# Kernel optimization log

Measured on AMD Instinct MI355X. Metric: run time of the kernel, lower is better.

The kernel has to match this reference:

```python
import jax, jax.numpy as jnp
import numpy as np

H = 16
DH = 64
THETA = 10000.0


def setup_inputs() -> dict:
    key = jax.random.key(0)
    ks = jax.random.split(key, 9)
    B, M, R = 4, 1024, 256
    d = H * DH
    s = 0.05
    return {
        "Pq": jax.random.normal(ks[0], (B, M, R), jnp.float32) * s,
        "Pk": jax.random.normal(ks[1], (B, M, R), jnp.float32) * s,
        "Pv": jax.random.normal(ks[2], (B, M, R), jnp.float32) * s,
        "Vq": jax.random.normal(ks[3], (R, d), jnp.float32) * s,
        "Vk": jax.random.normal(ks[4], (R, d), jnp.float32) * s,
        "Vv": jax.random.normal(ks[5], (R, d), jnp.float32) * s,
        "bq": jax.random.normal(ks[6], (d,), jnp.float32) * s,
        "bk": jax.random.normal(ks[7], (d,), jnp.float32) * s,
        "bv": jax.random.normal(ks[8], (d,), jnp.float32) * s,
        "attention_mask": jnp.ones((B, M), jnp.int32),
        "position_ids": jnp.tile(jnp.arange(M, dtype=jnp.int32), (B, 1)),
    }


def _rope_cos_sin(position_ids):
    # half-dim frequencies, matching the kernel's half-half rotation
    half = DH // 2
    inv_freq = 1.0 / (THETA ** (jnp.arange(0, half, dtype=jnp.float32) / half))
    ang = position_ids.astype(jnp.float32)[..., None] * inv_freq  # [B,M,half]
    return jnp.cos(ang), jnp.sin(ang)


def _rotate(x, cos, sin):
    # x: [B,H,M,dh]; cos/sin: [B,M,half] -> broadcast over heads
    half = DH // 2
    x0, x1 = x[..., :half], x[..., half:]
    c = cos[:, None, :, :]
    s = sin[:, None, :, :]
    return jnp.concatenate([x0 * c - x1 * s, x0 * s + x1 * c], axis=-1)


def reference(Pq, Pk, Pv, Vq, Vk, Vv, bq, bk, bv, attention_mask, position_ids):
    B, M, R = Pq.shape
    # reconstruct per-head Q/K/V from low-rank factors
    Vq3 = Vq.reshape(R, H, DH)
    Vk3 = Vk.reshape(R, H, DH)
    Vv3 = Vv.reshape(R, H, DH)
    q = jnp.einsum("bmr,rhd->bhmd", Pq, Vq3) + bq.reshape(H, DH)[None, :, None, :]
    k = jnp.einsum("bmr,rhd->bhmd", Pk, Vk3) + bk.reshape(H, DH)[None, :, None, :]
    v = jnp.einsum("bmr,rhd->bhmd", Pv, Vv3) + bv.reshape(H, DH)[None, :, None, :]
    cos, sin = _rope_cos_sin(position_ids)
    q = _rotate(q, cos, sin)
    k = _rotate(k, cos, sin)
    scale = 1.0 / jnp.sqrt(jnp.float32(DH))
    scores = jnp.einsum("bhmd,bhnd->bhmn", q, k) * scale  # [B,H,M,M]
    valid = attention_mask.astype(bool)
    pad = valid[:, None, :, None] & valid[:, None, None, :]
    scores = jnp.where(pad, scores, -jnp.inf)
    p = jax.nn.softmax(scores, axis=-1)
    out = jnp.einsum("bhmn,bhnd->bhmd", p, v)
    return out
```

## Files before the change

### kernel.cpp

```cpp
#include <hip/hip_runtime.h>
#include <hip/hip_bf16.h>
#include <math.h>

#define BB 4
#define MM 1024
#define RR 256
#define HH 16
#define DHH 64
#define DD (HH*DHH)

typedef __attribute__((ext_vector_type(8))) short short8;
typedef __attribute__((ext_vector_type(4))) float f32x4;

static __device__ __forceinline__ unsigned short f2bf(float x) {
    __hip_bfloat16 h = __float2bfloat16(x);
    return *(unsigned short*)&h;
}

#if defined(__has_builtin)
#  if __has_builtin(__builtin_amdgcn_exp2f)
#    define EXP2F(x) __builtin_amdgcn_exp2f(x)
#  endif
#endif
#ifndef EXP2F
#  define EXP2F(x) __expf((x) * 0.6931471805599453f)
#endif

static __device__ __forceinline__ unsigned pack_bf16_rh(float a, float b) {
    unsigned ua = __builtin_bit_cast(unsigned, a) + 0x8000u;
    unsigned ub = __builtin_bit_cast(unsigned, b) + 0x8000u;
    return __builtin_amdgcn_perm(ub, ua, 0x07060302u);
}

__global__ __launch_bounds__(256) void prep_kernel(
    const float* __restrict__ Vq, const float* __restrict__ Vk, const float* __restrict__ Vv,
    __hip_bfloat16* __restrict__ VTq, __hip_bfloat16* __restrict__ VTk,
    __hip_bfloat16* __restrict__ VTv)
{
    const int t   = threadIdx.x;
    const int z   = blockIdx.x / 256;
    const int rem = blockIdx.x % 256;
    const int r0  = (rem & 7) * 32;
    const int d0  = (rem >> 3) * 32;
    const float* V = (z == 0) ? Vq : (z == 1) ? Vk : Vv;
    __hip_bfloat16* VT = (z == 0) ? VTq : (z == 1) ? VTk : VTv;

    __shared__ __hip_bfloat16 Ts[32][33];
    {
        const int row = t >> 3;
        const int c4  = (t & 7) * 4;
        float4 f = *(const float4*)&V[(size_t)(r0 + row) * DD + d0 + c4];
        Ts[row][c4 + 0] = __float2bfloat16(f.x);
        Ts[row][c4 + 1] = __float2bfloat16(f.y);
        Ts[row][c4 + 2] = __float2bfloat16(f.z);
        Ts[row][c4 + 3] = __float2bfloat16(f.w);
    }
    __syncthreads();
    {
        const int orow = t >> 3;
        const int oc4  = (t & 7) * 4;
        union { unsigned short u[4]; uint2 v; } pk;
        #pragma unroll
        for (int i = 0; i < 4; ++i) pk.u[i] = *(unsigned short*)&Ts[oc4 + i][orow];
        *(uint2*)&VT[(size_t)(d0 + orow) * RR + r0 + oc4] = pk.v;
    }
}

__global__ __launch_bounds__(256) void svd_gemm(
    const float* __restrict__ Pq, const float* __restrict__ Pk, const float* __restrict__ Pv,
    const __hip_bfloat16* __restrict__ VTq, const __hip_bfloat16* __restrict__ VTk,
    const __hip_bfloat16* __restrict__ VTv,
    const float* __restrict__ bq, const float* __restrict__ bk, const float* __restrict__ bv,
    const int* __restrict__ pos_ids,
    __hip_bfloat16* __restrict__ qout, __hip_bfloat16* __restrict__ kout,
    __hip_bfloat16* __restrict__ vTout)
{
    const int which = blockIdx.z;
    const float* P           = (which == 0) ? Pq : (which == 1) ? Pk : Pv;
    const __hip_bfloat16* VT = (which == 0) ? VTq : (which == 1) ? VTk : VTv;
    const float* bias        = (which == 0) ? bq : (which == 1) ? bk : bv;

    const int hg  = blockIdx.y;
    const int bm0 = blockIdx.x * 64;
    const int b   = bm0 >> 10;
    const int m0  = bm0 & 1023;
    const int tid = threadIdx.x;
    const int lane = tid & 63;
    const int w    = tid >> 6;
    const int l15  = lane & 15;
    const int quad = lane >> 4;

    __shared__ alignas(16) short SM[(64 + 256) * 72];
    short* As = SM;
    short* Bs = SM + 64 * 72;

    f32x4 acc[16];
    #pragma unroll
    for (int dt = 0; dt < 16; ++dt) acc[dt] = (f32x4){0.f, 0.f, 0.f, 0.f};

    for (int kc = 0; kc < 4; ++kc) {
        #pragma unroll
        for (int i = 0; i < 4; ++i) {
            int u   = tid + i * 256;
            int row = u >> 4;
            int c4  = (u & 15) * 4;
            float4 f = *(const float4*)&P[(size_t)(bm0 + row) * RR + kc * 64 + c4];
            uint2 pk;
            pk.x = pack_bf16_rh(f.x, f.y);
            pk.y = pack_bf16_rh(f.z, f.w);
            *(uint2*)&As[row * 72 + c4] = pk;
        }
        #pragma unroll
        for (int i = 0; i < 8; ++i) {
            int u   = tid + i * 256;
            int row = u >> 3;
            int cg  = (u & 7) * 8;
            *(uint4*)&Bs[row * 72 + cg] =
                *(const uint4*)((const short*)VT + (size_t)(hg * 256 + row) * RR + kc * 64 + cg);
        }
        __syncthreads();

        #pragma unroll
        for (int ks = 0; ks < 2; ++ks) {
            short8 a = *(const short8*)&As[(w * 16 + l15) * 72 + ks * 32 + quad * 8];
            #pragma unroll
            for (int dt = 0; dt < 16; ++dt) {
                short8 bf = *(const short8*)&Bs[(dt * 16 + l15) * 72 + ks * 32 + quad * 8];
                acc[dt] = __builtin_amdgcn_mfma_f32_16x16x32_bf16(a, bf, acc[dt], 0, 0, 0);
            }
        }
        __syncthreads();
    }

    #pragma unroll
    for (int dt = 0; dt < 16; ++dt) {
        float bc = bias[hg * 256 + dt * 16 + l15];
        #pragma unroll
        for (int r = 0; r < 4; ++r) acc[dt][r] += bc;
    }

    if (which < 2) {
        __hip_bfloat16* out = (which == 0) ? qout : kout;
        int pm[4];
        #pragma unroll
        for (int r = 0; r < 4; ++r)
            pm[r] = pos_ids[bm0 + w * 16 + quad * 4 + r];
        float cB[2][4], sB[2][4];
        #pragma unroll
        for (int f2 = 0; f2 < 2; ++f2) {
            float invf = __powf(10000.0f, -(float)(f2 * 16 + l15) * (1.0f / 32.0f));
            #pragma unroll
            for (int r = 0; r < 4; ++r) {
                float ang = (float)pm[r] * invf;
                __sincosf(ang, &sB[f2][r], &cB[f2][r]);
            }
        }
        #pragma unroll
        for (int dt = 0; dt < 16; ++dt) {
            const int h  = hg * 4 + (dt >> 2);
            const int cd = (dt & 3) * 16 + l15;
            const int f2 = dt & 1;
            #pragma unroll
            for (int r = 0; r < 4; ++r) {
                float x  = acc[dt][r];
                float xp = acc[dt ^ 2][r];
                float c = cB[f2][r], s = sB[f2][r];
                float val = ((dt & 3) < 2) ? (x * c - xp * s) : (xp * s + x * c);
                int m = m0 + w * 16 + quad * 4 + r;
                out[(((size_t)b * HH + h) * MM + m) * DHH + cd] = __float2bfloat16(val);
            }
        }
    } else {
        short* Tt = SM;
        #pragma unroll
        for (int pp = 0; pp < 2; ++pp) {
            __syncthreads();
            #pragma unroll
            for (int dt2 = 0; dt2 < 8; ++dt2) {
                int dt = pp * 8 + dt2;
                uint2 pk;
                pk.x = pack_bf16_rh(acc[dt][0], acc[dt][1]);
                pk.y = pack_bf16_rh(acc[dt][2], acc[dt][3]);
                *(uint2*)&Tt[(dt2 * 16 + l15) * 72 + w * 16 + quad * 4] = pk;
            }
            __syncthreads();
            #pragma unroll
            for (int i = 0; i < 4; ++i) {
                int u   = tid + i * 256;
                int row = u >> 3;
                int seg = u & 7;
                int dl  = pp * 128 + row;
                int h   = hg * 4 + (dl >> 6);
                int din = dl & 63;
                *(uint4*)&vTout[(((size_t)b * HH + h) * DHH + din) * MM + m0 + seg * 8] =
                    *(const uint4*)&Tt[row * 72 + seg * 8];
            }
        }
    }
}

__global__ __launch_bounds__(256, 2) void attn_kernel(
    const __hip_bfloat16* __restrict__ q, const __hip_bfloat16* __restrict__ k,
    const __hip_bfloat16* __restrict__ vT,
    const int* __restrict__ mask, float* __restrict__ out)
{
    const int bh   = blockIdx.x & 63;
    const int qt   = blockIdx.x >> 6;
    const int b    = bh >> 4;
    const int tid  = threadIdx.x;
    const int lane = tid & 63;
    const int w    = tid >> 6;
    const int l15  = lane & 15;
    const int quad = lane >> 4;
    const int q0   = qt * 128;

    __shared__ alignas(16) __hip_bfloat16 Kt[128][72];
    __shared__ alignas(16) __hip_bfloat16 Vt[64][136];

    const short* kbase = (const short*)k  + (size_t)bh * MM * DHH;
    const short* vbase = (const short*)vT + (size_t)bh * DHH * MM;

    short8 qa[2][2];
    #pragma unroll
    for (int mt = 0; mt < 2; ++mt) {
        const short* qb = (const short*)q +
            ((size_t)bh * MM + q0 + w * 32 + mt * 16 + l15) * DHH + quad * 8;
        qa[mt][0] = *(const short8*)(qb);
        qa[mt][1] = *(const short8*)(qb + 32);
    }

    f32x4 Ot[2][4];
    #pragma unroll
    for (int mt = 0; mt < 2; ++mt)
        #pragma unroll
        for (int dt = 0; dt < 4; ++dt) Ot[mt][dt] = (f32x4){0.f, 0.f, 0.f, 0.f};
    float lsum[2] = {0.f, 0.f};

    const int* maskb = mask + b * MM;
    const int srcbase = (lane & 48) | ((lane & 48) >> 2);
    const float k2 = 0.125f * 1.44269504089f;

    for (int nc = 0; nc < MM / 128; ++nc) {
        const int n0 = nc * 128;
        #pragma unroll
        for (int pass = 0; pass < 4; ++pass) {
            int u   = tid + pass * 256;
            int row = u >> 3;
            int cg  = u & 7;
            *(uint4*)&Kt[row][cg * 8] =
                *(const uint4*)(kbase + (size_t)(n0 + row) * DHH + cg * 8);
        }
        #pragma unroll
        for (int pass = 0; pass < 4; ++pass) {
            int u   = tid + pass * 256;
            int row = u >> 4;
            int c   = u & 15;
            union { uint4 q4; uint2 h2[2]; } vld;
            vld.q4 = *(const uint4*)(vbase + (size_t)row * MM + n0 + c * 8);
            int g  = c >> 3;
            int c6 = c & 7;
            int base0 = g * 64 + (c6 >> 2) * 32 + (c6 & 1) * 16 + ((c6 >> 1) & 1) * 4;
            *(uint2*)&Vt[row][base0]     = vld.h2[0];
            *(uint2*)&Vt[row][base0 + 8] = vld.h2[1];
        }
        __syncthreads();

        unsigned long long bal0 = __ballot(maskb[n0 + lane] != 0);
        unsigned long long bal1 = __ballot(maskb[n0 + 64 + lane] != 0);

        f32x4 S[2][8];
        #pragma unroll
        for (int t = 0; t < 8; ++t) {
            const short* kr = (const short*)&Kt[t * 16 + l15][quad * 8];
            short8 ka0 = *(const short8*)(kr);
            short8 ka1 = *(const short8*)(kr + 32);
            #pragma unroll
            for (int mt = 0; mt < 2; ++mt) {
                f32x4 c = (f32x4){0.f, 0.f, 0.f, 0.f};
                c = __builtin_amdgcn_mfma_f32_16x16x32_bf16(ka0, qa[mt][0], c, 0, 0, 0);
                c = __builtin_amdgcn_mfma_f32_16x16x32_bf16(ka1, qa[mt][1], c, 0, 0, 0);
                S[mt][t] = c;
            }
        }

        #pragma unroll
        for (int t = 0; t < 8; ++t) {
            unsigned bits = (unsigned)((t < 4 ? bal0 : bal1) >> ((t & 3) * 16 + quad * 4));
            #pragma unroll
            for (int r = 0; r < 4; ++r) {
                float sb = ((bits >> r) & 1u) ? 0.0f : -1e30f;
                #pragma unroll
                for (int mt = 0; mt < 2; ++mt) {
                    float e = EXP2F(fmaf(S[mt][t][r], k2, sb));
                    lsum[mt] += e;
                    S[mt][t][r] = e;
                }
            }
        }

        short8 pa[2][4];
        #pragma unroll
        for (int mt = 0; mt < 2; ++mt)
            #pragma unroll
            for (int p = 0; p < 4; ++p) {
                union { unsigned u[4]; short8 s; } pk;
                pk.u[0] = pack_bf16_rh(S[mt][2*p][0],   S[mt][2*p][1]);
                pk.u[1] = pack_bf16_rh(S[mt][2*p][2],   S[mt][2*p][3]);
                pk.u[2] = pack_bf16_rh(S[mt][2*p+1][0], S[mt][2*p+1][1]);
                pk.u[3] = pack_bf16_rh(S[mt][2*p+1][2], S[mt][2*p+1][3]);
                pa[mt][p] = pk.s;
            }

        #pragma unroll
        for (int p = 0; p < 4; ++p) {
            #pragma unroll
            for (int dt = 0; dt < 4; ++dt) {
                short8 vb = *(const short8*)&Vt[dt * 16 + l15][p * 32 + quad * 8];
                #pragma unroll
                for (int mt = 0; mt < 2; ++mt)
                    Ot[mt][dt] = __builtin_amdgcn_mfma_f32_16x16x32_bf16(pa[mt][p], vb, Ot[mt][dt], 0, 0, 0);
            }
        }
        __syncthreads();
    }

    #pragma unroll
    for (int mt = 0; mt < 2; ++mt) {
        float s = lsum[mt];
        s += __shfl_xor(s, 16, 64);
        s += __shfl_xor(s, 32, 64);
        float inv = 1.0f / s;
        float* ob = out + ((size_t)bh * MM + q0 + w * 32 + mt * 16) * DHH;
        #pragma unroll
        for (int r = 0; r < 4; ++r) {
            float ir = __shfl(inv, srcbase + r, 64);
            #pragma unroll
            for (int dt = 0; dt < 4; ++dt)
                ob[(quad * 4 + r) * DHH + dt * 16 + l15] = Ot[mt][dt][r] * ir;
        }
    }
}

extern "C" void kernel_launch(void* const* d_in, const int* in_sizes, int n_in,
                              void* d_out, int out_size, void* d_ws, size_t ws_size,
                              hipStream_t stream) {
    const float* Pq = (const float*)d_in[0];
    const float* Pk = (const float*)d_in[1];
    const float* Pv = (const float*)d_in[2];
    const float* Vq = (const float*)d_in[3];
    const float* Vk = (const float*)d_in[4];
    const float* Vv = (const float*)d_in[5];
    const float* bq = (const float*)d_in[6];
    const float* bk = (const float*)d_in[7];
    const float* bv = (const float*)d_in[8];
    const int* mask = (const int*)d_in[9];
    const int* pos  = (const int*)d_in[10];
    float* out = (float*)d_out;

    const size_t qkv_elems = (size_t)BB * HH * MM * DHH;
    __hip_bfloat16* qb  = (__hip_bfloat16*)d_ws;
    __hip_bfloat16* kb  = qb + qkv_elems;
    __hip_bfloat16* vT  = kb + qkv_elems;
    __hip_bfloat16* VTq = vT + qkv_elems;
    __hip_bfloat16* VTk = VTq + (size_t)DD * RR;
    __hip_bfloat16* VTv = VTk + (size_t)DD * RR;

    prep_kernel<<<768, 256, 0, stream>>>(Vq, Vk, Vv, VTq, VTk, VTv);

    dim3 gG(BB * MM / 64, HH / 4, 3);
    svd_gemm<<<gG, 256, 0, stream>>>(Pq, Pk, Pv, VTq, VTk, VTv, bq, bk, bv, pos,
                                     qb, kb, vT);

    attn_kernel<<<BB * HH * (MM / 128), 256, 0, stream>>>(qb, kb, vT, mask, out);
}
```

Baseline: 156.4 us.

## Retile SVD projection GEMM to 128x128 tiles with A operands read straight into registers

Each block of the low-rank Q/K/V projection now covers 128 rows by 128 output columns (two heads) instead of 64 rows by 256 columns. The P operand is loaded from global memory, converted to bf16 and packed directly into MFMA A fragments, with no staging through LDS. Only the V^T tile is staged in shared memory, in two K chunks of 128 with separate accumulators that are summed at the end. The aim is fewer LDS round trips and barriers and more MFMAs per B fragment load. In exchange, each P row is read by twice as many blocks and register use per thread goes up.

```diff
diff --git a/kernel.cpp b/kernel.cpp
--- a/kernel.cpp
+++ b/kernel.cpp
@@ -81,7 +81,7 @@
     const float* bias        = (which == 0) ? bq : (which == 1) ? bk : bv;
 
     const int hg  = blockIdx.y;
-    const int bm0 = blockIdx.x * 64;
+    const int bm0 = blockIdx.x * 128;
     const int b   = bm0 >> 10;
     const int m0  = bm0 & 1023;
     const int tid = threadIdx.x;
@@ -90,111 +90,137 @@
     const int l15  = lane & 15;
     const int quad = lane >> 4;
 
-    __shared__ alignas(16) short SM[(64 + 256) * 72];
-    short* As = SM;
-    short* Bs = SM + 64 * 72;
+    __shared__ alignas(16) short Bs[128 * 136];
 
     f32x4 acc[16];
-    #pragma unroll
-    for (int dt = 0; dt < 16; ++dt) acc[dt] = (f32x4){0.f, 0.f, 0.f, 0.f};
-
-    for (int kc = 0; kc < 4; ++kc) {
-        #pragma unroll
-        for (int i = 0; i < 4; ++i) {
+    f32x4 acc2[16];
+    #pragma unroll
+    for (int dt = 0; dt < 16; ++dt) {
+        acc[dt]  = (f32x4){0.f, 0.f, 0.f, 0.f};
+        acc2[dt] = (f32x4){0.f, 0.f, 0.f, 0.f};
+    }
+
+    const float* prow0 = P + (size_t)(bm0 + w * 32 + l15) * RR;
+    const float* prow1 = P + (size_t)(bm0 + w * 32 + 16 + l15) * RR;
+
+    #pragma unroll
+    for (int kc = 0; kc < 2; ++kc) {
+        #pragma unroll
+        for (int i = 0; i < 8; ++i) {
             int u   = tid + i * 256;
             int row = u >> 4;
-            int c4  = (u & 15) * 4;
-            float4 f = *(const float4*)&P[(size_t)(bm0 + row) * RR + kc * 64 + c4];
+            int cg  = (u & 15) * 8;
+            *(uint4*)&Bs[row * 136 + cg] =
+                *(const uint4*)((const short*)VT + (size_t)(hg * 128 + row) * RR + kc * 128 + cg);
+        }
+        __syncthreads();
+
+        #pragma unroll
+        for (int ks = 0; ks < 4; ++ks) {
+            const int ko = kc * 128 + ks * 32 + quad * 8;
+            float4 a0lo = *(const float4*)(prow0 + ko);
+            float4 a0hi = *(const float4*)(prow0 + ko + 4);
+            float4 a1lo = *(const float4*)(prow1 + ko);
+            float4 a1hi = *(const float4*)(prow1 + ko + 4);
+            union { unsigned u[4]; short8 s; } pa0, pa1;
+            pa0.u[0] = pack_bf16_rh(a0lo.x, a0lo.y);
+            pa0.u[1] = pack_bf16_rh(a0lo.z, a0lo.w);
+            pa0.u[2] = pack_bf16_rh(a0hi.x, a0hi.y);
+            pa0.u[3] = pack_bf16_rh(a0hi.z, a0hi.w);
+            pa1.u[0] = pack_bf16_rh(a1lo.x, a1lo.y);
+            pa1.u[1] = pack_bf16_rh(a1lo.z, a1lo.w);
+            pa1.u[2] = pack_bf16_rh(a1hi.x, a1hi.y);
+            pa1.u[3] = pack_bf16_rh(a1hi.z, a1hi.w);
+
+            #pragma unroll
+            for (int dt = 0; dt < 8; ++dt) {
+                short8 bf = *(const short8*)&Bs[(dt * 16 + l15) * 136 + ks * 32 + quad * 8];
+                acc[kc * 8 + dt]  = __builtin_amdgcn_mfma_f32_16x16x32_bf16(pa0.s, bf, acc[kc * 8 + dt], 0, 0, 0);
+                acc2[kc * 8 + dt] = __builtin_amdgcn_mfma_f32_16x16x32_bf16(pa1.s, bf, acc2[kc * 8 + dt], 0, 0, 0);
+            }
+        }
+        __syncthreads();
+    }
+    #pragma unroll
+    for (int dt = 0; dt < 8; ++dt) {
+        #pragma unroll
+        for (int r = 0; r < 4; ++r) {
+            acc[dt][r]  += acc[8 + dt][r];
+            acc2[dt][r] += acc2[8 + dt][r];
+        }
+    }
+
+    #pragma unroll
+    for (int dt = 0; dt < 8; ++dt) {
+        float bc = bias[hg * 128 + dt * 16 + l15];
+        #pragma unroll
+        for (int r = 0; r < 4; ++r) { acc[dt][r] += bc; acc2[dt][r] += bc; }
+    }
+
+    if (which < 2) {
+        __hip_bfloat16* out = (which == 0) ? qout : kout;
+        int pm0[4], pm1[4];
+        #pragma unroll
+        for (int r = 0; r < 4; ++r) {
+            pm0[r] = pos_ids[bm0 + w * 32 + quad * 4 + r];
+            pm1[r] = pos_ids[bm0 + w * 32 + 16 + quad * 4 + r];
+        }
+        float cB[2][2][4], sB[2][2][4];
+        #pragma unroll
+        for (int f2 = 0; f2 < 2; ++f2) {
+            float invf = __powf(10000.0f, -(float)(f2 * 16 + l15) * (1.0f / 32.0f));
+            #pragma unroll
+            for (int r = 0; r < 4; ++r) {
+                __sincosf((float)pm0[r] * invf, &sB[f2][0][r], &cB[f2][0][r]);
+                __sincosf((float)pm1[r] * invf, &sB[f2][1][r], &cB[f2][1][r]);
+            }
+        }
+        #pragma unroll
+        for (int dt = 0; dt < 8; ++dt) {
+            const int h  = hg * 2 + (dt >> 2);
+            const int cd = (dt & 3) * 16 + l15;
+            const int f2 = dt & 1;
+            #pragma unroll
+            for (int r = 0; r < 4; ++r) {
+                {
+                    float x  = acc[dt][r], xp = acc[dt ^ 2][r];
+                    float c = cB[f2][0][r], s = sB[f2][0][r];
+                    float val = ((dt & 3) < 2) ? (x * c - xp * s) : (xp * s + x * c);
+                    int m = m0 + w * 32 + quad * 4 + r;
+                    out[(((size_t)b * HH + h) * MM + m) * DHH + cd] = __float2bfloat16(val);
+                }
+                {
+                    float x  = acc2[dt][r], xp = acc2[dt ^ 2][r];
+                    float c = cB[f2][1][r], s = sB[f2][1][r];
+                    float val = ((dt & 3) < 2) ? (x * c - xp * s) : (xp * s + x * c);
+                    int m = m0 + w * 32 + 16 + quad * 4 + r;
+                    out[(((size_t)b * HH + h) * MM + m) * DHH + cd] = __float2bfloat16(val);
+                }
+            }
+        }
+    } else {
+        short* Tt = Bs;
+        __syncthreads();
+        #pragma unroll
+        for (int dt = 0; dt < 8; ++dt) {
             uint2 pk;
-            pk.x = pack_bf16_rh(f.x, f.y);
-            pk.y = pack_bf16_rh(f.z, f.w);
-            *(uint2*)&As[row * 72 + c4] = pk;
-        }
+            pk.x = pack_bf16_rh(acc[dt][0], acc[dt][1]);
+            pk.y = pack_bf16_rh(acc[dt][2], acc[dt][3]);
+            *(uint2*)&Tt[(dt * 16 + l15) * 136 + w * 32 + quad * 4] = pk;
+            pk.x = pack_bf16_rh(acc2[dt][0], acc2[dt][1]);
+            pk.y = pack_bf16_rh(acc2[dt][2], acc2[dt][3]);
+            *(uint2*)&Tt[(dt * 16 + l15) * 136 + w * 32 + 16 + quad * 4] = pk;
+        }
+        __syncthreads();
         #pragma unroll
         for (int i = 0; i < 8; ++i) {
             int u   = tid + i * 256;
-            int row = u >> 3;
-            int cg  = (u & 7) * 8;
-            *(uint4*)&Bs[row * 72 + cg] =
-                *(const uint4*)((const short*)VT + (size_t)(hg * 256 + row) * RR + kc * 64 + cg);
-        }
-        __syncthreads();
-
-        #pragma unroll
-        for (int ks = 0; ks < 2; ++ks) {
-            short8 a = *(const short8*)&As[(w * 16 + l15) * 72 + ks * 32 + quad * 8];
-            #pragma unroll
-            for (int dt = 0; dt < 16; ++dt) {
-                short8 bf = *(const short8*)&Bs[(dt * 16 + l15) * 72 + ks * 32 + quad * 8];
-                acc[dt] = __builtin_amdgcn_mfma_f32_16x16x32_bf16(a, bf, acc[dt], 0, 0, 0);
-            }
-        }
-        __syncthreads();
-    }
-
-    #pragma unroll
-    for (int dt = 0; dt < 16; ++dt) {
-        float bc = bias[hg * 256 + dt * 16 + l15];
-        #pragma unroll
-        for (int r = 0; r < 4; ++r) acc[dt][r] += bc;
-    }
-
-    if (which < 2) {
-        __hip_bfloat16* out = (which == 0) ? qout : kout;
-        int pm[4];
-        #pragma unroll
-        for (int r = 0; r < 4; ++r)
-            pm[r] = pos_ids[bm0 + w * 16 + quad * 4 + r];
-        float cB[2][4], sB[2][4];
-        #pragma unroll
-        for (int f2 = 0; f2 < 2; ++f2) {
-            float invf = __powf(10000.0f, -(float)(f2 * 16 + l15) * (1.0f / 32.0f));
-            #pragma unroll
-            for (int r = 0; r < 4; ++r) {
-                float ang = (float)pm[r] * invf;
-                __sincosf(ang, &sB[f2][r], &cB[f2][r]);
-            }
-        }
-        #pragma unroll
-        for (int dt = 0; dt < 16; ++dt) {
-            const int h  = hg * 4 + (dt >> 2);
-            const int cd = (dt & 3) * 16 + l15;
-            const int f2 = dt & 1;
-            #pragma unroll
-            for (int r = 0; r < 4; ++r) {
-                float x  = acc[dt][r];
-                float xp = acc[dt ^ 2][r];
-                float c = cB[f2][r], s = sB[f2][r];
-                float val = ((dt & 3) < 2) ? (x * c - xp * s) : (xp * s + x * c);
-                int m = m0 + w * 16 + quad * 4 + r;
-                out[(((size_t)b * HH + h) * MM + m) * DHH + cd] = __float2bfloat16(val);
-            }
-        }
-    } else {
-        short* Tt = SM;
-        #pragma unroll
-        for (int pp = 0; pp < 2; ++pp) {
-            __syncthreads();
-            #pragma unroll
-            for (int dt2 = 0; dt2 < 8; ++dt2) {
-                int dt = pp * 8 + dt2;
-                uint2 pk;
-                pk.x = pack_bf16_rh(acc[dt][0], acc[dt][1]);
-                pk.y = pack_bf16_rh(acc[dt][2], acc[dt][3]);
-                *(uint2*)&Tt[(dt2 * 16 + l15) * 72 + w * 16 + quad * 4] = pk;
-            }
-            __syncthreads();
-            #pragma unroll
-            for (int i = 0; i < 4; ++i) {
-                int u   = tid + i * 256;
-                int row = u >> 3;
-                int seg = u & 7;
-                int dl  = pp * 128 + row;
-                int h   = hg * 4 + (dl >> 6);
-                int din = dl & 63;
-                *(uint4*)&vTout[(((size_t)b * HH + h) * DHH + din) * MM + m0 + seg * 8] =
-                    *(const uint4*)&Tt[row * 72 + seg * 8];
-            }
+            int row = u >> 4;
+            int seg = u & 15;
+            int h   = hg * 2 + (row >> 6);
+            int din = row & 63;
+            *(uint4*)&vTout[(((size_t)b * HH + h) * DHH + din) * MM + m0 + seg * 8] =
+                *(const uint4*)&Tt[row * 136 + seg * 8];
         }
     }
 }
@@ -367,7 +393,7 @@
 
     prep_kernel<<<768, 256, 0, stream>>>(Vq, Vk, Vv, VTq, VTk, VTv);
 
-    dim3 gG(BB * MM / 64, HH / 4, 3);
+    dim3 gG(BB * MM / 128, HH / 2, 3);
     svd_gemm<<<gG, 256, 0, stream>>>(Pq, Pk, Pv, VTq, VTk, VTv, bq, bk, bv, pos,
                                      qb, kb, vT);
 
```

New measurement: 144.0 us. 7.9% less time.

## Split attention KV across warps and halve GEMM tile width for more blocks

Applied to the files above, without the earlier changes.

The attention kernel now processes 64 query rows per block instead of 128. The four warps are split into two query halves and two key halves, and the key-half partial outputs and row sums are combined through shared memory at the end, doubling the block count. The projection GEMM now covers two heads per block, loads P rows straight from global memory into registers, and stages the rotated Q/K output through shared memory for coalesced 16-byte stores. The aim is better occupancy and wave fill, at the cost of redundant K/V tile loads per query row and an extra reduction step.

```diff
diff --git a/kernel.cpp b/kernel.cpp
--- a/kernel.cpp
+++ b/kernel.cpp
@@ -11,11 +11,6 @@
 
 typedef __attribute__((ext_vector_type(8))) short short8;
 typedef __attribute__((ext_vector_type(4))) float f32x4;
-
-static __device__ __forceinline__ unsigned short f2bf(float x) {
-    __hip_bfloat16 h = __float2bfloat16(x);
-    return *(unsigned short*)&h;
-}
 
 #if defined(__has_builtin)
 #  if __has_builtin(__builtin_amdgcn_exp2f)
@@ -30,6 +25,9 @@
     unsigned ua = __builtin_bit_cast(unsigned, a) + 0x8000u;
     unsigned ub = __builtin_bit_cast(unsigned, b) + 0x8000u;
     return __builtin_amdgcn_perm(ub, ua, 0x07060302u);
+}
+static __device__ __forceinline__ unsigned short bf_rh(float a) {
+    return (unsigned short)((__builtin_bit_cast(unsigned, a) + 0x8000u) >> 16);
 }
 
 __global__ __launch_bounds__(256) void prep_kernel(
@@ -66,7 +64,7 @@
     }
 }
 
-__global__ __launch_bounds__(256) void svd_gemm(
+__global__ __launch_bounds__(256, 4) void svd_gemm(
     const float* __restrict__ Pq, const float* __restrict__ Pk, const float* __restrict__ Pv,
     const __hip_bfloat16* __restrict__ VTq, const __hip_bfloat16* __restrict__ VTk,
     const __hip_bfloat16* __restrict__ VTv,
@@ -90,51 +88,48 @@
     const int l15  = lane & 15;
     const int quad = lane >> 4;
 
-    __shared__ alignas(16) short SM[(64 + 256) * 72];
-    short* As = SM;
-    short* Bs = SM + 64 * 72;
-
-    f32x4 acc[16];
-    #pragma unroll
-    for (int dt = 0; dt < 16; ++dt) acc[dt] = (f32x4){0.f, 0.f, 0.f, 0.f};
-
+    __shared__ alignas(16) short Bs[128 * 72];
+
+    f32x4 acc[8];
+    #pragma unroll
+    for (int dt = 0; dt < 8; ++dt) acc[dt] = (f32x4){0.f, 0.f, 0.f, 0.f};
+
+    const float* prow = P + (size_t)(bm0 + w * 16 + l15) * RR;
+
+    #pragma unroll
     for (int kc = 0; kc < 4; ++kc) {
         #pragma unroll
         for (int i = 0; i < 4; ++i) {
-            int u   = tid + i * 256;
-            int row = u >> 4;
-            int c4  = (u & 15) * 4;
-            float4 f = *(const float4*)&P[(size_t)(bm0 + row) * RR + kc * 64 + c4];
-            uint2 pk;
-            pk.x = pack_bf16_rh(f.x, f.y);
-            pk.y = pack_bf16_rh(f.z, f.w);
-            *(uint2*)&As[row * 72 + c4] = pk;
-        }
-        #pragma unroll
-        for (int i = 0; i < 8; ++i) {
             int u   = tid + i * 256;
             int row = u >> 3;
             int cg  = (u & 7) * 8;
             *(uint4*)&Bs[row * 72 + cg] =
-                *(const uint4*)((const short*)VT + (size_t)(hg * 256 + row) * RR + kc * 64 + cg);
+                *(const uint4*)((const short*)VT + (size_t)(hg * 128 + row) * RR + kc * 64 + cg);
         }
         __syncthreads();
 
         #pragma unroll
         for (int ks = 0; ks < 2; ++ks) {
-            short8 a = *(const short8*)&As[(w * 16 + l15) * 72 + ks * 32 + quad * 8];
-            #pragma unroll
-            for (int dt = 0; dt < 16; ++dt) {
+            const int ko = kc * 64 + ks * 32 + quad * 8;
+            float4 alo = *(const float4*)(prow + ko);
+            float4 ahi = *(const float4*)(prow + ko + 4);
+            union { unsigned u[4]; short8 s; } pa;
+            pa.u[0] = pack_bf16_rh(alo.x, alo.y);
+            pa.u[1] = pack_bf16_rh(alo.z, alo.w);
+            pa.u[2] = pack_bf16_rh(ahi.x, ahi.y);
+            pa.u[3] = pack_bf16_rh(ahi.z, ahi.w);
+            #pragma unroll
+            for (int dt = 0; dt < 8; ++dt) {
                 short8 bf = *(const short8*)&Bs[(dt * 16 + l15) * 72 + ks * 32 + quad * 8];
-                acc[dt] = __builtin_amdgcn_mfma_f32_16x16x32_bf16(a, bf, acc[dt], 0, 0, 0);
-            }
-        }
-        __syncthreads();
-    }
-
-    #pragma unroll
-    for (int dt = 0; dt < 16; ++dt) {
-        float bc = bias[hg * 256 + dt * 16 + l15];
+                acc[dt] = __builtin_amdgcn_mfma_f32_16x16x32_bf16(pa.s, bf, acc[dt], 0, 0, 0);
+            }
+        }
+        __syncthreads();
+    }
+
+    #pragma unroll
+    for (int dt = 0; dt < 8; ++dt) {
+        float bc = bias[hg * 128 + dt * 16 + l15];
         #pragma unroll
         for (int r = 0; r < 4; ++r) acc[dt][r] += bc;
     }
@@ -143,76 +138,77 @@
         __hip_bfloat16* out = (which == 0) ? qout : kout;
         int pm[4];
         #pragma unroll
-        for (int r = 0; r < 4; ++r)
-            pm[r] = pos_ids[bm0 + w * 16 + quad * 4 + r];
+        for (int r = 0; r < 4; ++r) pm[r] = pos_ids[bm0 + w * 16 + quad * 4 + r];
         float cB[2][4], sB[2][4];
         #pragma unroll
         for (int f2 = 0; f2 < 2; ++f2) {
             float invf = __powf(10000.0f, -(float)(f2 * 16 + l15) * (1.0f / 32.0f));
             #pragma unroll
+            for (int r = 0; r < 4; ++r)
+                __sincosf((float)pm[r] * invf, &sB[f2][r], &cB[f2][r]);
+        }
+        short* Ls = Bs;
+        #pragma unroll
+        for (int dt = 0; dt < 8; ++dt) {
+            const int f2 = dt & 1;
+            #pragma unroll
             for (int r = 0; r < 4; ++r) {
-                float ang = (float)pm[r] * invf;
-                __sincosf(ang, &sB[f2][r], &cB[f2][r]);
-            }
-        }
-        #pragma unroll
-        for (int dt = 0; dt < 16; ++dt) {
-            const int h  = hg * 4 + (dt >> 2);
-            const int cd = (dt & 3) * 16 + l15;
-            const int f2 = dt & 1;
-            #pragma unroll
-            for (int r = 0; r < 4; ++r) {
-                float x  = acc[dt][r];
-                float xp = acc[dt ^ 2][r];
+                float x  = acc[dt][r], xp = acc[dt ^ 2][r];
                 float c = cB[f2][r], s = sB[f2][r];
                 float val = ((dt & 3) < 2) ? (x * c - xp * s) : (xp * s + x * c);
-                int m = m0 + w * 16 + quad * 4 + r;
-                out[(((size_t)b * HH + h) * MM + m) * DHH + cd] = __float2bfloat16(val);
-            }
+                Ls[(w * 16 + quad * 4 + r) * 136 + dt * 16 + l15] = (short)bf_rh(val);
+            }
+        }
+        __syncthreads();
+        #pragma unroll
+        for (int i = 0; i < 4; ++i) {
+            int u   = tid + i * 256;
+            int ml  = u >> 4;
+            int hh  = (u >> 3) & 1;
+            int seg = u & 7;
+            *(uint4*)&out[(((size_t)b * HH + hg * 2 + hh) * MM + m0 + ml) * DHH + seg * 8] =
+                *(const uint4*)&Ls[ml * 136 + hh * 64 + seg * 8];
         }
     } else {
-        short* Tt = SM;
-        #pragma unroll
-        for (int pp = 0; pp < 2; ++pp) {
-            __syncthreads();
-            #pragma unroll
-            for (int dt2 = 0; dt2 < 8; ++dt2) {
-                int dt = pp * 8 + dt2;
-                uint2 pk;
-                pk.x = pack_bf16_rh(acc[dt][0], acc[dt][1]);
-                pk.y = pack_bf16_rh(acc[dt][2], acc[dt][3]);
-                *(uint2*)&Tt[(dt2 * 16 + l15) * 72 + w * 16 + quad * 4] = pk;
-            }
-            __syncthreads();
-            #pragma unroll
-            for (int i = 0; i < 4; ++i) {
-                int u   = tid + i * 256;
-                int row = u >> 3;
-                int seg = u & 7;
-                int dl  = pp * 128 + row;
-                int h   = hg * 4 + (dl >> 6);
-                int din = dl & 63;
-                *(uint4*)&vTout[(((size_t)b * HH + h) * DHH + din) * MM + m0 + seg * 8] =
-                    *(const uint4*)&Tt[row * 72 + seg * 8];
-            }
-        }
-    }
-}
-
-__global__ __launch_bounds__(256, 2) void attn_kernel(
+        short* Tt = Bs;
+        #pragma unroll
+        for (int dt = 0; dt < 8; ++dt) {
+            uint2 pk;
+            pk.x = pack_bf16_rh(acc[dt][0], acc[dt][1]);
+            pk.y = pack_bf16_rh(acc[dt][2], acc[dt][3]);
+            *(uint2*)&Tt[(dt * 16 + l15) * 72 + w * 16 + quad * 4] = pk;
+        }
+        __syncthreads();
+        #pragma unroll
+        for (int i = 0; i < 4; ++i) {
+            int u   = tid + i * 256;
+            int row = u >> 3;
+            int seg = u & 7;
+            int h   = hg * 2 + (row >> 6);
+            int din = row & 63;
+            *(uint4*)&vTout[(((size_t)b * HH + h) * DHH + din) * MM + m0 + seg * 8] =
+                *(const uint4*)&Tt[row * 72 + seg * 8];
+        }
+    }
+}
+
+__global__ __launch_bounds__(256, 4) void attn_kernel(
     const __hip_bfloat16* __restrict__ q, const __hip_bfloat16* __restrict__ k,
     const __hip_bfloat16* __restrict__ vT,
     const int* __restrict__ mask, float* __restrict__ out)
 {
-    const int bh   = blockIdx.x & 63;
-    const int qt   = blockIdx.x >> 6;
-    const int b    = bh >> 4;
-    const int tid  = threadIdx.x;
-    const int lane = tid & 63;
-    const int w    = tid >> 6;
-    const int l15  = lane & 15;
-    const int quad = lane >> 4;
-    const int q0   = qt * 128;
+    const int bh    = blockIdx.x & 63;
+    const int qt    = blockIdx.x >> 6;
+    const int b     = bh >> 4;
+    const int tid   = threadIdx.x;
+    const int lane  = tid & 63;
+    const int w     = tid >> 6;
+    const int mhalf = w & 1;
+    const int khalf = w >> 1;
+    const int l15   = lane & 15;
+    const int quad  = lane >> 4;
+    const int q0    = qt * 64;
+    const int koff  = khalf * 64;
 
     __shared__ alignas(16) __hip_bfloat16 Kt[128][72];
     __shared__ alignas(16) __hip_bfloat16 Vt[64][136];
@@ -224,7 +220,7 @@
     #pragma unroll
     for (int mt = 0; mt < 2; ++mt) {
         const short* qb = (const short*)q +
-            ((size_t)bh * MM + q0 + w * 32 + mt * 16 + l15) * DHH + quad * 8;
+            ((size_t)bh * MM + q0 + mhalf * 32 + mt * 16 + l15) * DHH + quad * 8;
         qa[mt][0] = *(const short8*)(qb);
         qa[mt][1] = *(const short8*)(qb + 32);
     }
@@ -265,13 +261,12 @@
         }
         __syncthreads();
 
-        unsigned long long bal0 = __ballot(maskb[n0 + lane] != 0);
-        unsigned long long bal1 = __ballot(maskb[n0 + 64 + lane] != 0);
-
-        f32x4 S[2][8];
-        #pragma unroll
-        for (int t = 0; t < 8; ++t) {
-            const short* kr = (const short*)&Kt[t * 16 + l15][quad * 8];
+        unsigned long long bal = __ballot(maskb[n0 + koff + lane] != 0);
+
+        f32x4 S[2][4];
+        #pragma unroll
+        for (int t = 0; t < 4; ++t) {
+            const short* kr = (const short*)&Kt[koff + t * 16 + l15][quad * 8];
             short8 ka0 = *(const short8*)(kr);
             short8 ka1 = *(const short8*)(kr + 32);
             #pragma unroll
@@ -284,8 +279,8 @@
         }
 
         #pragma unroll
-        for (int t = 0; t < 8; ++t) {
-            unsigned bits = (unsigned)((t < 4 ? bal0 : bal1) >> ((t & 3) * 16 + quad * 4));
+        for (int t = 0; t < 4; ++t) {
+            unsigned bits = (unsigned)(bal >> (t * 16 + quad * 4));
             #pragma unroll
             for (int r = 0; r < 4; ++r) {
                 float sb = ((bits >> r) & 1u) ? 0.0f : -1e30f;
@@ -298,11 +293,11 @@
             }
         }
 
-        short8 pa[2][4];
+        short8 pa[2][2];
         #pragma unroll
         for (int mt = 0; mt < 2; ++mt)
             #pragma unroll
-            for (int p = 0; p < 4; ++p) {
+            for (int p = 0; p < 2; ++p) {
                 union { unsigned u[4]; short8 s; } pk;
                 pk.u[0] = pack_bf16_rh(S[mt][2*p][0],   S[mt][2*p][1]);
                 pk.u[1] = pack_bf16_rh(S[mt][2*p][2],   S[mt][2*p][3]);
@@ -312,10 +307,10 @@
             }
 
         #pragma unroll
-        for (int p = 0; p < 4; ++p) {
+        for (int p = 0; p < 2; ++p) {
             #pragma unroll
             for (int dt = 0; dt < 4; ++dt) {
-                short8 vb = *(const short8*)&Vt[dt * 16 + l15][p * 32 + quad * 8];
+                short8 vb = *(const short8*)&Vt[dt * 16 + l15][koff + p * 32 + quad * 8];
                 #pragma unroll
                 for (int mt = 0; mt < 2; ++mt)
                     Ot[mt][dt] = __builtin_amdgcn_mfma_f32_16x16x32_bf16(pa[mt][p], vb, Ot[mt][dt], 0, 0, 0);
@@ -324,19 +319,44 @@
         __syncthreads();
     }
 
-    #pragma unroll
-    for (int mt = 0; mt < 2; ++mt) {
-        float s = lsum[mt];
-        s += __shfl_xor(s, 16, 64);
-        s += __shfl_xor(s, 32, 64);
-        float inv = 1.0f / s;
-        float* ob = out + ((size_t)bh * MM + q0 + w * 32 + mt * 16) * DHH;
-        #pragma unroll
-        for (int r = 0; r < 4; ++r) {
-            float ir = __shfl(inv, srcbase + r, 64);
+    float* C = (float*)&Kt[0][0];
+    const int cb = (mhalf * 64 + lane) * 34;
+    if (khalf == 1) {
+        #pragma unroll
+        for (int mt = 0; mt < 2; ++mt) {
             #pragma unroll
             for (int dt = 0; dt < 4; ++dt)
-                ob[(quad * 4 + r) * DHH + dt * 16 + l15] = Ot[mt][dt][r] * ir;
+                #pragma unroll
+                for (int r = 0; r < 4; ++r)
+                    C[cb + mt * 16 + dt * 4 + r] = Ot[mt][dt][r];
+            C[cb + 32 + mt] = lsum[mt];
+        }
+    }
+    __syncthreads();
+    if (khalf == 0) {
+        #pragma unroll
+        for (int mt = 0; mt < 2; ++mt) {
+            #pragma unroll
+            for (int dt = 0; dt < 4; ++dt)
+                #pragma unroll
+                for (int r = 0; r < 4; ++r)
+                    Ot[mt][dt][r] += C[cb + mt * 16 + dt * 4 + r];
+            lsum[mt] += C[cb + 32 + mt];
+        }
+        #pragma unroll
+        for (int mt = 0; mt < 2; ++mt) {
+            float s = lsum[mt];
+            s += __shfl_xor(s, 16, 64);
+            s += __shfl_xor(s, 32, 64);
+            float inv = 1.0f / s;
+            float* ob = out + ((size_t)bh * MM + q0 + mhalf * 32 + mt * 16) * DHH;
+            #pragma unroll
+            for (int r = 0; r < 4; ++r) {
+                float ir = __shfl(inv, srcbase + r, 64);
+                #pragma unroll
+                for (int dt = 0; dt < 4; ++dt)
+                    ob[(quad * 4 + r) * DHH + dt * 16 + l15] = Ot[mt][dt][r] * ir;
+            }
         }
     }
 }
@@ -367,9 +387,9 @@
 
     prep_kernel<<<768, 256, 0, stream>>>(Vq, Vk, Vv, VTq, VTk, VTv);
 
-    dim3 gG(BB * MM / 64, HH / 4, 3);
+    dim3 gG(BB * MM / 64, HH / 2, 3);
     svd_gemm<<<gG, 256, 0, stream>>>(Pq, Pk, Pv, VTq, VTk, VTv, bq, bk, bv, pos,
                                      qb, kb, vT);
 
-    attn_kernel<<<BB * HH * (MM / 128), 256, 0, stream>>>(qb, kb, vT, mask, out);
-}
+    attn_kernel<<<BB * HH * (MM / 64), 256, 0, stream>>>(qb, kb, vT, mask, out);
+}
```

Result: faster. 139.1 us (-11.0%).
